# Kernel tuning notes

Measured on AMD Instinct MI355X. Metric: run time of the kernel, lower is better.

Reference implementation:

```python
import jax, jax.numpy as jnp
import numpy as np

N_NODES = 50000
N_EDGES = 800000
F_IN = 64
HID = 64
N_CLASSES = 10


def setup_inputs() -> dict:
    key = jax.random.key(0)
    ks = jax.random.split(key, 16)
    features = jax.random.normal(ks[0], (N_NODES, F_IN), dtype=jnp.float32)
    edge_indicies = jax.random.randint(ks[1], (2, N_EDGES), 0, N_NODES, dtype=jnp.int64)
    s = 1.0 / np.sqrt(HID)
    params = {}
    # three GINConv MLPs: Linear(in,64) -> ReLU -> Linear(64,64)
    for i in range(3):
        d_in = F_IN if i == 0 else HID
        si = 1.0 / np.sqrt(d_in)
        params[f"W1_{i}"] = jax.random.uniform(ks[2 + 4 * i], (d_in, HID), jnp.float32, -si, si)
        params[f"b1_{i}"] = jax.random.uniform(ks[3 + 4 * i], (HID,), jnp.float32, -si, si)
        params[f"W2_{i}"] = jax.random.uniform(ks[4 + 4 * i], (HID, HID), jnp.float32, -s, s)
        params[f"b2_{i}"] = jax.random.uniform(ks[5 + 4 * i], (HID,), jnp.float32, -s, s)
    params["W_lin"] = jax.random.uniform(ks[14], (HID, N_CLASSES), jnp.float32, -s, s)
    params["b_lin"] = jax.random.uniform(ks[15], (N_CLASSES,), jnp.float32, -s, s)
    return {"features": features, "edge_indicies": edge_indicies, **params}


def _gin_conv(x, src, dst, W1, b1, W2, b2):
    # aggregate: sum_{j in N(i)} x_j  (messages flow src -> dst), eps = 0
    agg = jax.ops.segment_sum(x[src], dst, num_segments=N_NODES)
    h = agg + x  # (1 + eps) * x + aggregate, eps=0
    # MLP: Linear -> ReLU -> Linear
    return jax.nn.relu(h @ W1 + b1) @ W2 + b2


def reference(features, edge_indicies,
              W1_0, b1_0, W2_0, b2_0,
              W1_1, b1_1, W2_1, b2_1,
              W1_2, b1_2, W2_2, b2_2,
              W_lin, b_lin):
    src, dst = edge_indicies[0], edge_indicies[1]
    x = jax.nn.relu(_gin_conv(features, src, dst, W1_0, b1_0, W2_0, b2_0))
    x = jax.nn.relu(_gin_conv(x, src, dst, W1_1, b1_1, W2_1, b2_1))
    x = jax.nn.relu(_gin_conv(x, src, dst, W1_2, b1_2, W2_2, b2_2))
    return x @ W_lin + b_lin
```

## Files before the change

kernel.cpp:

```cpp
#include <hip/hip_runtime.h>
#include <hip/hip_bf16.h>

#define FDIM 64
#define BNODES 64
#define CHUNK 4096
#define HP 72
#define GCAP 2048

typedef short bf16x8 __attribute__((ext_vector_type(8)));
typedef float f32x4 __attribute__((ext_vector_type(4)));

__device__ __forceinline__ unsigned short f2bf(float f) {
    unsigned int u = __float_as_uint(f);
    unsigned int r = (u + 0x7fffu + ((u >> 16) & 1u)) >> 16;
    return (unsigned short)r;
}
__device__ __forceinline__ float bflo(unsigned int p) { return __uint_as_float(p << 16); }
__device__ __forceinline__ float bfhi(unsigned int p) { return __uint_as_float(p & 0xffff0000u); }

__global__ __launch_bounds__(256) void cast_prep_hist(const float* __restrict__ x,
                                                      unsigned short* __restrict__ xb, int n4,
                                                      int ncast,
                                                      const float* __restrict__ W10,
                                                      const float* __restrict__ W20,
                                                      const float* __restrict__ W11,
                                                      const float* __restrict__ W21,
                                                      const float* __restrict__ W12,
                                                      const float* __restrict__ W22,
                                                      unsigned short* __restrict__ wt,
                                                      const int* __restrict__ dst,
                                                      int* __restrict__ hist,
                                                      int n_edges, int nbuck) {
    int tid = threadIdx.x;
    if (blockIdx.x < (unsigned)ncast) {
        int i = blockIdx.x * 256 + tid;
        if (i < n4) {
            float4 v = ((const float4*)x)[i];
            uint2 o;
            o.x = (unsigned int)f2bf(v.x) | ((unsigned int)f2bf(v.y) << 16);
            o.y = (unsigned int)f2bf(v.z) | ((unsigned int)f2bf(v.w) << 16);
            ((uint2*)xb)[i] = o;
        }
        return;
    }
    if (blockIdx.x < (unsigned)(ncast + 6)) {
        __shared__ unsigned short s[64 * 64];
        int wsel = blockIdx.x - ncast;
        const float* W;
        switch (wsel) {
            case 0: W = W10; break;
            case 1: W = W20; break;
            case 2: W = W11; break;
            case 3: W = W21; break;
            case 4: W = W12; break;
            default: W = W22; break;
        }
#pragma unroll
        for (int p = 0; p < 4; p++) {
            int idx = tid + p * 256;
            int k = idx >> 4;
            int n0 = (idx & 15) * 4;
            float4 v = ((const float4*)W)[idx];
            s[(n0 + 0) * 64 + k] = f2bf(v.x);
            s[(n0 + 1) * 64 + k] = f2bf(v.y);
            s[(n0 + 2) * 64 + k] = f2bf(v.z);
            s[(n0 + 3) * 64 + k] = f2bf(v.w);
        }
        __syncthreads();
        uint4* o = (uint4*)(wt + (size_t)wsel * 4096);
#pragma unroll
        for (int p = 0; p < 2; p++) {
            int idx = tid + p * 256;
            o[idx] = ((uint4*)s)[idx];
        }
        return;
    }
    {
        __shared__ int lh[1024];
        int chunk = blockIdx.x - ncast - 6;
        for (int i = tid; i < nbuck; i += 256) lh[i] = 0;
        __syncthreads();
        int beg = chunk * CHUNK;
        int end = min(beg + CHUNK, n_edges);
        for (int e = beg + tid; e < end; e += 256)
            atomicAdd(&lh[dst[e] >> 6], 1);
        __syncthreads();
        for (int i = tid; i < nbuck; i += 256)
            hist[(size_t)chunk * nbuck + i] = lh[i];
    }
}

__global__ __launch_bounds__(256) void scan_chunks(const int* __restrict__ hist,
                                                   int* __restrict__ chunk_off,
                                                   int* __restrict__ bucket_total,
                                                   int nchunks, int nbuck) {
    __shared__ int s[256];
    int b = blockIdx.x;
    int t = threadIdx.x;
    int v = (t < nchunks) ? hist[(size_t)t * nbuck + b] : 0;
    s[t] = v;
    __syncthreads();
    for (int off = 1; off < 256; off <<= 1) {
        int u = (t >= off) ? s[t - off] : 0;
        __syncthreads();
        s[t] += u;
        __syncthreads();
    }
    if (t < nchunks) chunk_off[(size_t)t * nbuck + b] = s[t] - v;
    if (t == 255) bucket_total[b] = s[255];
}

__global__ __launch_bounds__(1024) void scan_buckets(const int* __restrict__ bucket_total,
                                                     int* __restrict__ bucket_start,
                                                     int* __restrict__ row_ptr,
                                                     int nbuck, int n_nodes, int n_edges) {
    __shared__ int s[1024];
    int t = threadIdx.x;
    int v = (t < nbuck) ? bucket_total[t] : 0;
    s[t] = v;
    __syncthreads();
    for (int off = 1; off < 1024; off <<= 1) {
        int u = (t >= off) ? s[t - off] : 0;
        __syncthreads();
        s[t] += u;
        __syncthreads();
    }
    if (t < nbuck) bucket_start[t] = s[t] - v;
    if (t == 0) { bucket_start[nbuck] = n_edges; row_ptr[n_nodes] = n_edges; }
}

__global__ __launch_bounds__(256) void bucket_fill(const int* __restrict__ src,
                                                   const int* __restrict__ dst,
                                                   const int* __restrict__ bucket_start,
                                                   const int* __restrict__ chunk_off,
                                                   unsigned int* __restrict__ packed,
                                                   int n_edges, int nbuck) {
    __shared__ int cur[1024];
    int chunk = blockIdx.x;
    for (int i = threadIdx.x; i < nbuck; i += 256)
        cur[i] = bucket_start[i] + chunk_off[(size_t)chunk * nbuck + i];
    __syncthreads();
    int beg = chunk * CHUNK;
    int end = min(beg + CHUNK, n_edges);
    for (int e = beg + threadIdx.x; e < end; e += 256) {
        int d = dst[e];
        int b = d >> 6;
        int pos = atomicAdd(&cur[b], 1);
        packed[pos] = (unsigned int)src[e] | ((unsigned int)(d & 63) << 16);
    }
}

__global__ __launch_bounds__(256) void sort_bucket(const unsigned int* __restrict__ packed,
                                                   const int* __restrict__ bucket_start,
                                                   int* __restrict__ src_sorted,
                                                   int* __restrict__ row_ptr, int n_nodes) {
    __shared__ int cnt[BNODES];
    __shared__ int cur[BNODES];
    int b = blockIdx.x;
    int beg = bucket_start[b], end = bucket_start[b + 1];
    if (threadIdx.x < BNODES) cnt[threadIdx.x] = 0;
    __syncthreads();
    for (int e = beg + threadIdx.x; e < end; e += 256)
        atomicAdd(&cnt[packed[e] >> 16], 1);
    __syncthreads();
    if (threadIdx.x < 64) {
        int v = cnt[threadIdx.x];
        int inc = v;
#pragma unroll
        for (int off = 1; off < 64; off <<= 1) {
            int u = __shfl_up(inc, off, 64);
            if (threadIdx.x >= off) inc += u;
        }
        cur[threadIdx.x] = beg + inc - v;
        int node = b * BNODES + threadIdx.x;
        if (node < n_nodes) row_ptr[node] = beg + inc - v;
    }
    __syncthreads();
    for (int e = beg + threadIdx.x; e < end; e += 256) {
        unsigned int p = packed[e];
        int pos = atomicAdd(&cur[p >> 16], 1);
        src_sorted[pos] = (int)(p & 0xFFFFu);
    }
}

__global__ __launch_bounds__(256) void gather_bf16(const unsigned short* __restrict__ xb,
                                                   const int* __restrict__ row_ptr,
                                                   const int* __restrict__ src_sorted,
                                                   unsigned short* __restrict__ hb,
                                                   int n_nodes) {
    __shared__ int sidx[GCAP];
    int base = blockIdx.x * 32;
    int ebeg = row_ptr[base];
    int eend = row_ptr[min(base + 32, n_nodes)];
    int total = eend - ebeg;
    int cnt = min(total, GCAP);
    for (int i = threadIdx.x; i < cnt; i += 256) sidx[i] = src_sorted[ebeg + i];
    __syncthreads();

    int t = threadIdx.x;
    int node = base + (t >> 3);
    if (node >= n_nodes) return;
    int c = (t & 7) * 8;
    int dbeg = row_ptr[node] - ebeg;
    int dend = row_ptr[node + 1] - ebeg;
    int dmid = (total <= GCAP) ? dend : min(dend, cnt);

    float acc[8];
    {
        uint4 v = *(const uint4*)(xb + (size_t)node * FDIM + c);
        acc[0] = bflo(v.x); acc[1] = bfhi(v.x);
        acc[2] = bflo(v.y); acc[3] = bfhi(v.y);
        acc[4] = bflo(v.z); acc[5] = bfhi(v.z);
        acc[6] = bflo(v.w); acc[7] = bfhi(v.w);
    }

    int e = dbeg;
    for (; e + 7 < dmid; e += 8) {
        int s[8];
#pragma unroll
        for (int j = 0; j < 8; j++) s[j] = sidx[e + j];
        uint4 v[8];
#pragma unroll
        for (int j = 0; j < 8; j++) v[j] = *(const uint4*)(xb + (size_t)s[j] * FDIM + c);
#pragma unroll
        for (int j = 0; j < 8; j++) {
            acc[0] += bflo(v[j].x); acc[1] += bfhi(v[j].x);
            acc[2] += bflo(v[j].y); acc[3] += bfhi(v[j].y);
            acc[4] += bflo(v[j].z); acc[5] += bfhi(v[j].z);
            acc[6] += bflo(v[j].w); acc[7] += bfhi(v[j].w);
        }
    }
    if (e + 3 < dmid) {
        int s[4];
#pragma unroll
        for (int j = 0; j < 4; j++) s[j] = sidx[e + j];
        uint4 v[4];
#pragma unroll
        for (int j = 0; j < 4; j++) v[j] = *(const uint4*)(xb + (size_t)s[j] * FDIM + c);
#pragma unroll
        for (int j = 0; j < 4; j++) {
            acc[0] += bflo(v[j].x); acc[1] += bfhi(v[j].x);
            acc[2] += bflo(v[j].y); acc[3] += bfhi(v[j].y);
            acc[4] += bflo(v[j].z); acc[5] += bfhi(v[j].z);
            acc[6] += bflo(v[j].w); acc[7] += bfhi(v[j].w);
        }
        e += 4;
    }
    for (; e < dmid; e++) {
        uint4 v = *(const uint4*)(xb + (size_t)sidx[e] * FDIM + c);
        acc[0] += bflo(v.x); acc[1] += bfhi(v.x);
        acc[2] += bflo(v.y); acc[3] += bfhi(v.y);
        acc[4] += bflo(v.z); acc[5] += bfhi(v.z);
        acc[6] += bflo(v.w); acc[7] += bfhi(v.w);
    }
    for (; e < dend; e++) {
        uint4 v = *(const uint4*)(xb + (size_t)src_sorted[ebeg + e] * FDIM + c);
        acc[0] += bflo(v.x); acc[1] += bfhi(v.x);
        acc[2] += bflo(v.y); acc[3] += bfhi(v.y);
        acc[4] += bflo(v.z); acc[5] += bfhi(v.z);
        acc[6] += bflo(v.w); acc[7] += bfhi(v.w);
    }

    uint4 p;
    p.x = (unsigned int)f2bf(acc[0]) | ((unsigned int)f2bf(acc[1]) << 16);
    p.y = (unsigned int)f2bf(acc[2]) | ((unsigned int)f2bf(acc[3]) << 16);
    p.z = (unsigned int)f2bf(acc[4]) | ((unsigned int)f2bf(acc[5]) << 16);
    p.w = (unsigned int)f2bf(acc[6]) | ((unsigned int)f2bf(acc[7]) << 16);
    *(uint4*)(hb + (size_t)node * FDIM + c) = p;
}

__global__ __launch_bounds__(256) void mlp_mfma(const unsigned short* __restrict__ xb,
        const unsigned short* __restrict__ wt1, const float* __restrict__ b1,
        const unsigned short* __restrict__ wt2, const float* __restrict__ b2,
        const float* __restrict__ Wl, const float* __restrict__ bl,
        unsigned short* __restrict__ y, float* __restrict__ out,
        int n_nodes, int do_final) {
    __shared__ unsigned short sH[64 * HP];
    __shared__ unsigned short sW1t[64 * HP];
    __shared__ unsigned short sW2t[64 * HP];
    __shared__ float sb1[FDIM], sb2[FDIM];
    __shared__ float sWl[FDIM * 10];
    __shared__ float sbl[16];

    int tid = threadIdx.x;
    int base = blockIdx.x * 64;

    {
        const uint4* w1g = (const uint4*)wt1;
        const uint4* w2g = (const uint4*)wt2;
#pragma unroll
        for (int p = 0; p < 2; p++) {
            int idx = tid + p * 256;
            int r = idx >> 3, q = idx & 7;
            *(uint4*)(&sW1t[r * HP + q * 8]) = w1g[idx];
            *(uint4*)(&sW2t[r * HP + q * 8]) = w2g[idx];
        }
    }
    if (tid < FDIM) { sb1[tid] = b1[tid]; sb2[tid] = b2[tid]; }
    if (do_final) {
        for (int i = tid; i < FDIM * 10; i += 256) sWl[i] = Wl[i];
        if (tid < 10) sbl[tid] = bl[tid];
    }
#pragma unroll
    for (int p = 0; p < 2; p++) {
        int idx = tid + p * 256;
        int r = idx >> 3, q = idx & 7;
        uint4 v = make_uint4(0u, 0u, 0u, 0u);
        if (base + r < n_nodes) v = *(const uint4*)(xb + (size_t)(base + r) * FDIM + q * 8);
        *(uint4*)(&sH[r * HP + q * 8]) = v;
    }
    __syncthreads();

    int w = tid >> 6;
    int lane = tid & 63;
    int qd = lane >> 4;
    int m = lane & 15;
    int arow = (w * 16 + m) * HP;

    f32x4 acc[4];

    {
        bf16x8 a0 = *(bf16x8*)(&sH[arow + qd * 8]);
        bf16x8 a1 = *(bf16x8*)(&sH[arow + 32 + qd * 8]);
#pragma unroll
        for (int t = 0; t < 4; t++) {
            float bias = sb1[t * 16 + m];
            acc[t] = (f32x4){bias, bias, bias, bias};
            bf16x8 bA = *(bf16x8*)(&sW1t[(t * 16 + m) * HP + qd * 8]);
            bf16x8 bB = *(bf16x8*)(&sW1t[(t * 16 + m) * HP + 32 + qd * 8]);
            acc[t] = __builtin_amdgcn_mfma_f32_16x16x32_bf16(a0, bA, acc[t], 0, 0, 0);
            acc[t] = __builtin_amdgcn_mfma_f32_16x16x32_bf16(a1, bB, acc[t], 0, 0, 0);
        }
#pragma unroll
        for (int t = 0; t < 4; t++)
#pragma unroll
            for (int r = 0; r < 4; r++)
                sH[(w * 16 + qd * 4 + r) * HP + t * 16 + m] = f2bf(fmaxf(acc[t][r], 0.f));
    }

    {
        bf16x8 a0 = *(bf16x8*)(&sH[arow + qd * 8]);
        bf16x8 a1 = *(bf16x8*)(&sH[arow + 32 + qd * 8]);
#pragma unroll
        for (int t = 0; t < 4; t++) {
            float bias = sb2[t * 16 + m];
            acc[t] = (f32x4){bias, bias, bias, bias};
            bf16x8 bA = *(bf16x8*)(&sW2t[(t * 16 + m) * HP + qd * 8]);
            bf16x8 bB = *(bf16x8*)(&sW2t[(t * 16 + m) * HP + 32 + qd * 8]);
            acc[t] = __builtin_amdgcn_mfma_f32_16x16x32_bf16(a0, bA, acc[t], 0, 0, 0);
            acc[t] = __builtin_amdgcn_mfma_f32_16x16x32_bf16(a1, bB, acc[t], 0, 0, 0);
        }
#pragma unroll
        for (int t = 0; t < 4; t++)
#pragma unroll
            for (int r = 0; r < 4; r++)
                sH[(w * 16 + qd * 4 + r) * HP + t * 16 + m] = f2bf(fmaxf(acc[t][r], 0.f));
    }
    __syncthreads();

    if (!do_final) {
#pragma unroll
        for (int p = 0; p < 2; p++) {
            int idx = tid + p * 256;
            int r = idx >> 3, q = idx & 7;
            if (base + r < n_nodes)
                *(uint4*)(y + (size_t)(base + r) * FDIM + q * 8) = *(uint4*)(&sH[r * HP + q * 8]);
        }
    } else {
        for (int i = tid; i < 64 * 10; i += 256) {
            int nl = i / 10, cc = i % 10;
            int node = base + nl;
            if (node < n_nodes) {
                float s = sbl[cc];
#pragma unroll
                for (int k0 = 0; k0 < FDIM; k0 += 4) {
                    uint2 hp = *(uint2*)(&sH[nl * HP + k0]);
                    s += bflo(hp.x) * sWl[(k0 + 0) * 10 + cc] + bfhi(hp.x) * sWl[(k0 + 1) * 10 + cc]
                       + bflo(hp.y) * sWl[(k0 + 2) * 10 + cc] + bfhi(hp.y) * sWl[(k0 + 3) * 10 + cc];
                }
                out[(size_t)node * 10 + cc] = s;
            }
        }
    }
}

extern "C" void kernel_launch(void* const* d_in, const int* in_sizes, int n_in,
                              void* d_out, int out_size, void* d_ws, size_t ws_size,
                              hipStream_t stream) {
    const float* features = (const float*)d_in[0];
    const int* edges = (const int*)d_in[1];
    int n_nodes = in_sizes[0] / FDIM;
    int n_edges = in_sizes[1] / 2;
    const int* src = edges;
    const int* dst = edges + n_edges;

    int nbuck = (n_nodes + BNODES - 1) / BNODES;
    int nchunks = (n_edges + CHUNK - 1) / CHUNK;

    int* hist = (int*)d_ws;
    int* chunk_off = hist + (size_t)nchunks * nbuck;
    int* bucket_total = chunk_off + (size_t)nchunks * nbuck;
    int* bucket_start = bucket_total + nbuck;
    int* row_ptr = bucket_start + nbuck + 1;
    unsigned int* packed = (unsigned int*)(row_ptr + n_nodes + 1);
    int* src_sorted = (int*)(packed + n_edges);
    size_t int_elems = 2 * (size_t)nchunks * nbuck + 2 * (size_t)nbuck + 2
                       + (size_t)n_nodes + 2 * (size_t)n_edges;
    int_elems = (int_elems + 3) & ~(size_t)3;
    size_t buf_elems = (size_t)n_nodes * FDIM;
    unsigned short* hb  = (unsigned short*)((int*)d_ws + int_elems);
    unsigned short* xb0 = hb + buf_elems;
    unsigned short* yA  = xb0 + buf_elems;
    unsigned short* yB  = yA + buf_elems;
    unsigned short* wt  = yB + buf_elems;

    dim3 bs(256);
    int n4 = (int)(buf_elems / 4);
    int ncast = (n4 + 255) / 256;
    dim3 gs_cph(ncast + 6 + nchunks);
    dim3 gs_gather((n_nodes + 31) / 32);
    dim3 gs_tile((n_nodes + 63) / 64);

    cast_prep_hist<<<gs_cph, bs, 0, stream>>>(features, xb0, n4, ncast,
                                              (const float*)d_in[2], (const float*)d_in[4],
                                              (const float*)d_in[6], (const float*)d_in[8],
                                              (const float*)d_in[10], (const float*)d_in[12], wt,
                                              dst, hist, n_edges, nbuck);

    scan_chunks<<<nbuck, 256, 0, stream>>>(hist, chunk_off, bucket_total, nchunks, nbuck);
    scan_buckets<<<1, 1024, 0, stream>>>(bucket_total, bucket_start, row_ptr, nbuck, n_nodes, n_edges);
    bucket_fill<<<nchunks, 256, 0, stream>>>(src, dst, bucket_start, chunk_off, packed, n_edges, nbuck);
    sort_bucket<<<nbuck, 256, 0, stream>>>(packed, bucket_start, src_sorted, row_ptr, n_nodes);

    const float* Wl = (const float*)d_in[14];
    const float* bl = (const float*)d_in[15];
    const unsigned short* x_cur = xb0;
    unsigned short* outs[3] = {yA, yB, yA};
    for (int conv = 0; conv < 3; conv++) {
        const float* b1 = (const float*)d_in[3 + 4 * conv];
        const float* b2 = (const float*)d_in[5 + 4 * conv];
        const unsigned short* wt1 = wt + (size_t)(2 * conv) * 4096;
        const unsigned short* wt2 = wt + (size_t)(2 * conv + 1) * 4096;
        int fin = (conv == 2) ? 1 : 0;

        gather_bf16<<<gs_gather, bs, 0, stream>>>(x_cur, row_ptr, src_sorted, hb, n_nodes);
        mlp_mfma<<<gs_tile, bs, 0, stream>>>(hb, wt1, b1, wt2, b2, Wl, bl,
                                             outs[conv], (float*)d_out, n_nodes, fin);
        x_cur = outs[conv];
    }
}
```

Baseline: 195.6 us.

## Fuse bucket sort with first-layer neighbor gather in one kernel

Merges the per-bucket counting sort and the first GIN layer's bf16 neighbor aggregation into a single kernel with 512 threads per block. The bucket's packed edges and sorted source indices are staged in shared memory, so the first gather reads indices from LDS instead of re-reading src_sorted from global memory, and one kernel launch is removed. The cost is larger per-block shared memory and a fallback path for oversized buckets, and the gather for each bucket now runs with only 64 nodes per block.

```diff
diff --git a/kernel.cpp b/kernel.cpp
--- a/kernel.cpp
+++ b/kernel.cpp
@@ -6,6 +6,7 @@
 #define CHUNK 4096
 #define HP 72
 #define GCAP 2048
+#define SGT 512
 
 typedef short bf16x8 __attribute__((ext_vector_type(8)));
 typedef float f32x4 __attribute__((ext_vector_type(4)));
@@ -150,37 +151,137 @@
     }
 }
 
-__global__ __launch_bounds__(256) void sort_bucket(const unsigned int* __restrict__ packed,
+__global__ __launch_bounds__(SGT) void sort_gather(const unsigned int* __restrict__ packed,
                                                    const int* __restrict__ bucket_start,
+                                                   const unsigned short* __restrict__ xb,
                                                    int* __restrict__ src_sorted,
-                                                   int* __restrict__ row_ptr, int n_nodes) {
+                                                   int* __restrict__ row_ptr,
+                                                   unsigned short* __restrict__ hb,
+                                                   int n_nodes) {
+    __shared__ unsigned int spk[GCAP];
+    __shared__ int sidx[GCAP];
     __shared__ int cnt[BNODES];
+    __shared__ int nbeg[BNODES];
     __shared__ int cur[BNODES];
     int b = blockIdx.x;
-    int beg = bucket_start[b], end = bucket_start[b + 1];
-    if (threadIdx.x < BNODES) cnt[threadIdx.x] = 0;
-    __syncthreads();
-    for (int e = beg + threadIdx.x; e < end; e += 256)
-        atomicAdd(&cnt[packed[e] >> 16], 1);
-    __syncthreads();
-    if (threadIdx.x < 64) {
-        int v = cnt[threadIdx.x];
+    int tid = threadIdx.x;
+    int ebeg = bucket_start[b], eend = bucket_start[b + 1];
+    int total = eend - ebeg;
+    bool fits = (total <= GCAP);
+    if (tid < BNODES) cnt[tid] = 0;
+    if (fits)
+        for (int i = tid; i < total; i += SGT) spk[i] = packed[ebeg + i];
+    __syncthreads();
+    if (fits) {
+        for (int i = tid; i < total; i += SGT) atomicAdd(&cnt[spk[i] >> 16], 1);
+    } else {
+        for (int e = ebeg + tid; e < eend; e += SGT) atomicAdd(&cnt[packed[e] >> 16], 1);
+    }
+    __syncthreads();
+    if (tid < 64) {
+        int v = cnt[tid];
         int inc = v;
 #pragma unroll
         for (int off = 1; off < 64; off <<= 1) {
             int u = __shfl_up(inc, off, 64);
-            if (threadIdx.x >= off) inc += u;
-        }
-        cur[threadIdx.x] = beg + inc - v;
-        int node = b * BNODES + threadIdx.x;
-        if (node < n_nodes) row_ptr[node] = beg + inc - v;
-    }
-    __syncthreads();
-    for (int e = beg + threadIdx.x; e < end; e += 256) {
-        unsigned int p = packed[e];
-        int pos = atomicAdd(&cur[p >> 16], 1);
-        src_sorted[pos] = (int)(p & 0xFFFFu);
-    }
+            if (tid >= off) inc += u;
+        }
+        int ex = inc - v;
+        nbeg[tid] = ex;
+        cur[tid] = ex;
+        int node = b * BNODES + tid;
+        if (node < n_nodes) row_ptr[node] = ebeg + ex;
+    }
+    __syncthreads();
+    if (fits) {
+        for (int i = tid; i < total; i += SGT) {
+            unsigned int p = spk[i];
+            int pos = atomicAdd(&cur[p >> 16], 1);
+            int s = (int)(p & 0xFFFFu);
+            sidx[pos] = s;
+            src_sorted[ebeg + pos] = s;
+        }
+    } else {
+        for (int e = ebeg + tid; e < eend; e += SGT) {
+            unsigned int p = packed[e];
+            int pos = atomicAdd(&cur[p >> 16], 1);
+            src_sorted[ebeg + pos] = (int)(p & 0xFFFFu);
+        }
+    }
+    __syncthreads();
+
+    int nl = tid >> 3;
+    int node = b * BNODES + nl;
+    if (node >= n_nodes) return;
+    int c = (tid & 7) * 8;
+    int dbeg = nbeg[nl];
+    int dend = dbeg + cnt[nl];
+
+    float acc[8];
+    {
+        uint4 v = *(const uint4*)(xb + (size_t)node * FDIM + c);
+        acc[0] = bflo(v.x); acc[1] = bfhi(v.x);
+        acc[2] = bflo(v.y); acc[3] = bfhi(v.y);
+        acc[4] = bflo(v.z); acc[5] = bfhi(v.z);
+        acc[6] = bflo(v.w); acc[7] = bfhi(v.w);
+    }
+
+    if (fits) {
+        int e = dbeg;
+        for (; e + 7 < dend; e += 8) {
+            int s[8];
+#pragma unroll
+            for (int j = 0; j < 8; j++) s[j] = sidx[e + j];
+            uint4 v[8];
+#pragma unroll
+            for (int j = 0; j < 8; j++) v[j] = *(const uint4*)(xb + (size_t)s[j] * FDIM + c);
+#pragma unroll
+            for (int j = 0; j < 8; j++) {
+                acc[0] += bflo(v[j].x); acc[1] += bfhi(v[j].x);
+                acc[2] += bflo(v[j].y); acc[3] += bfhi(v[j].y);
+                acc[4] += bflo(v[j].z); acc[5] += bfhi(v[j].z);
+                acc[6] += bflo(v[j].w); acc[7] += bfhi(v[j].w);
+            }
+        }
+        if (e + 3 < dend) {
+            int s[4];
+#pragma unroll
+            for (int j = 0; j < 4; j++) s[j] = sidx[e + j];
+            uint4 v[4];
+#pragma unroll
+            for (int j = 0; j < 4; j++) v[j] = *(const uint4*)(xb + (size_t)s[j] * FDIM + c);
+#pragma unroll
+            for (int j = 0; j < 4; j++) {
+                acc[0] += bflo(v[j].x); acc[1] += bfhi(v[j].x);
+                acc[2] += bflo(v[j].y); acc[3] += bfhi(v[j].y);
+                acc[4] += bflo(v[j].z); acc[5] += bfhi(v[j].z);
+                acc[6] += bflo(v[j].w); acc[7] += bfhi(v[j].w);
+            }
+            e += 4;
+        }
+        for (; e < dend; e++) {
+            uint4 v = *(const uint4*)(xb + (size_t)sidx[e] * FDIM + c);
+            acc[0] += bflo(v.x); acc[1] += bfhi(v.x);
+            acc[2] += bflo(v.y); acc[3] += bfhi(v.y);
+            acc[4] += bflo(v.z); acc[5] += bfhi(v.z);
+            acc[6] += bflo(v.w); acc[7] += bfhi(v.w);
+        }
+    } else {
+        for (int e = dbeg; e < dend; e++) {
+            uint4 v = *(const uint4*)(xb + (size_t)src_sorted[ebeg + e] * FDIM + c);
+            acc[0] += bflo(v.x); acc[1] += bfhi(v.x);
+            acc[2] += bflo(v.y); acc[3] += bfhi(v.y);
+            acc[4] += bflo(v.z); acc[5] += bfhi(v.z);
+            acc[6] += bflo(v.w); acc[7] += bfhi(v.w);
+        }
+    }
+
+    uint4 p;
+    p.x = (unsigned int)f2bf(acc[0]) | ((unsigned int)f2bf(acc[1]) << 16);
+    p.y = (unsigned int)f2bf(acc[2]) | ((unsigned int)f2bf(acc[3]) << 16);
+    p.z = (unsigned int)f2bf(acc[4]) | ((unsigned int)f2bf(acc[5]) << 16);
+    p.w = (unsigned int)f2bf(acc[6]) | ((unsigned int)f2bf(acc[7]) << 16);
+    *(uint4*)(hb + (size_t)node * FDIM + c) = p;
 }
 
 __global__ __launch_bounds__(256) void gather_bf16(const unsigned short* __restrict__ xb,
@@ -430,13 +531,19 @@
     scan_chunks<<<nbuck, 256, 0, stream>>>(hist, chunk_off, bucket_total, nchunks, nbuck);
     scan_buckets<<<1, 1024, 0, stream>>>(bucket_total, bucket_start, row_ptr, nbuck, n_nodes, n_edges);
     bucket_fill<<<nchunks, 256, 0, stream>>>(src, dst, bucket_start, chunk_off, packed, n_edges, nbuck);
-    sort_bucket<<<nbuck, 256, 0, stream>>>(packed, bucket_start, src_sorted, row_ptr, n_nodes);
 
     const float* Wl = (const float*)d_in[14];
     const float* bl = (const float*)d_in[15];
-    const unsigned short* x_cur = xb0;
-    unsigned short* outs[3] = {yA, yB, yA};
-    for (int conv = 0; conv < 3; conv++) {
+
+    sort_gather<<<nbuck, SGT, 0, stream>>>(packed, bucket_start, xb0,
+                                           src_sorted, row_ptr, hb, n_nodes);
+    mlp_mfma<<<gs_tile, bs, 0, stream>>>(hb, wt, (const float*)d_in[3],
+                                         wt + 4096, (const float*)d_in[5], Wl, bl,
+                                         yA, (float*)d_out, n_nodes, 0);
+
+    const unsigned short* x_cur = yA;
+    unsigned short* outs2[2] = {yB, yA};
+    for (int conv = 1; conv < 3; conv++) {
         const float* b1 = (const float*)d_in[3 + 4 * conv];
         const float* b2 = (const float*)d_in[5 + 4 * conv];
         const unsigned short* wt1 = wt + (size_t)(2 * conv) * 4096;
@@ -445,7 +552,7 @@
 
         gather_bf16<<<gs_gather, bs, 0, stream>>>(x_cur, row_ptr, src_sorted, hb, n_nodes);
         mlp_mfma<<<gs_tile, bs, 0, stream>>>(hb, wt1, b1, wt2, b2, Wl, bl,
-                                             outs[conv], (float*)d_out, n_nodes, fin);
-        x_cur = outs[conv];
-    }
-}
+                                             outs2[conv - 1], (float*)d_out, n_nodes, fin);
+        x_cur = outs2[conv - 1];
+    }
+}
```

After: 193.9 us, median of 2. Within noise of the previous version (-0.9%).
